# Optimization experiments

Measured on AMD Instinct MI355X. Metric: run time of the kernel, lower is better.

Reference implementation:

```python
import jax, jax.numpy as jnp
import numpy as np

H, W = 256, 192           # cfg.input_img_shape
INF = 9999.0
B, V = 64, 100000


def setup_inputs() -> dict:
    key = jax.random.key(0)
    k1, k2, k3 = jax.random.split(key, 3)
    sdf = jax.random.normal(k1, (B, V), dtype=jnp.float32)
    # pixel coords spanning slightly beyond the image so some verts are invalid
    uv = jax.random.uniform(k2, (B, V, 2), dtype=jnp.float32)
    cloth_meshes = uv * jnp.array([W * 1.1, H * 1.1], jnp.float32) - jnp.array([W * 0.05, H * 0.05], jnp.float32)
    parse_gt = jax.random.randint(k3, (B, H, W), 0, 2).astype(jnp.int32)
    return {
        "sdf": sdf,
        "cloth_meshes": cloth_meshes,
        "parse_gt": parse_gt,
        "sdf_thresh": jnp.ones((1,), jnp.float32),
        "cloth_meshes_unposed": jnp.zeros((1, 1, 3), jnp.float32),
        "parse_valid": jnp.ones((B, 1, 1), jnp.float32),
        "dist_thresh": jnp.ones((1,), jnp.float32),
        "v_template": jnp.zeros((1, 3), jnp.float32),
    }


def reference(sdf, cloth_meshes, parse_gt, sdf_thresh, cloth_meshes_unposed, parse_valid, dist_thresh, v_template):
    b = sdf.shape[0]
    hw = H * W
    x = cloth_meshes[:, :, 0].astype(jnp.int32)
    y = cloth_meshes[:, :, 1].astype(jnp.int32)
    is_valid = (x >= 0) & (x < W) & (y >= 0) & (y < H)
    idx = jnp.where(is_valid, y * W + x, 0)                      # [B,V]
    min_sdf = jnp.where(is_valid, sdf, INF)
    max_sdf = jnp.where(is_valid, sdf, -INF)
    # single flattened segment reduce over B*H*W segments (scatter_min/max)
    flat_idx = (idx + jnp.arange(b, dtype=jnp.int32)[:, None] * hw).reshape(-1)
    pmin = jax.ops.segment_min(min_sdf.reshape(-1), flat_idx, num_segments=b * hw).reshape(b, H, W)
    pmax = jax.ops.segment_max(max_sdf.reshape(-1), flat_idx, num_segments=b * hw).reshape(b, H, W)
    # empty / all-invalid pixels: torch init was +/-INF -> replace
    pmin = jnp.where(pmin >= INF, 0.0, pmin)
    pmax = jnp.where(pmax <= -INF, sdf_thresh[0], pmax)
    pos_mask = (parse_gt == 1).astype(sdf.dtype)
    neg_mask = (parse_gt == 0).astype(sdf.dtype)
    loss_pos = jnp.abs(pmin) * pos_mask * parse_valid
    loss_neg = jnp.abs(pmax - sdf_thresh[0]) * neg_mask * parse_valid
    loss = loss_pos.mean((1, 2)) + loss_neg.mean((1, 2))
    cloth_exist = (pos_mask.sum((1, 2)) > 0).astype(sdf.dtype)
    return loss * cloth_exist
```

## Files before the change

### kernel.cpp

```cpp
#include <hip/hip_runtime.h>


#define HH 256
#define WW 192
#define HW (HH * WW)
#define NB 64
#define NV 100000
#define NS 4
#define RANGE (HW / NS)
#define NC 8
#define CHUNK (NV / NC)
#define F4B (NV / 4 / NC)
#define CAP 3000

__device__ __forceinline__ unsigned fkey(float f) {
    unsigned u = __float_as_uint(f);
    return (u & 0x80000000u) ? ~u : (u | 0x80000000u);
}
__device__ __forceinline__ float funkey(unsigned k) {
    unsigned u = (k & 0x80000000u) ? (k ^ 0x80000000u) : ~k;
    return __uint_as_float(u);
}
__device__ __forceinline__ unsigned key18(float f) {
    unsigned k = fkey(f);
    if (k >= 0xFFFFE000u) return 0x3FFFFu;
    return (k + 0x2000u) >> 14;
}

__global__ __launch_bounds__(512) void bin_kernel(
        const float4* __restrict__ sdf4,
        const float4* __restrict__ mesh4,
        unsigned* __restrict__ cnt,
        unsigned* __restrict__ records) {
    __shared__ unsigned lcur[NS];
    const int b = blockIdx.x >> 3;
    const int c = blockIdx.x & 7;
    const int tid = threadIdx.x;
    if (tid < NS) lcur[tid] = 0;
    __syncthreads();

    const float4* sbase = sdf4  + (size_t)b * (NV / 4) + (size_t)c * F4B;
    const float4* mbase = mesh4 + (size_t)b * (NV / 2) + (size_t)c * F4B * 2;
    unsigned* rbase = records + (size_t)(b * NC + c) * NS * CAP;

    for (int g = tid; g < F4B; g += 512) {
        float4 s4 = sbase[g];
        float4 ma = mbase[2 * g];
        float4 mb = mbase[2 * g + 1];
        float xs[4] = {ma.x, ma.z, mb.x, mb.z};
        float ys[4] = {ma.y, ma.w, mb.y, mb.w};
        float ss[4] = {s4.x, s4.y, s4.z, s4.w};
        #pragma unroll
        for (int j = 0; j < 4; ++j) {
            int x = (int)xs[j];
            int y = (int)ys[j];
            if ((unsigned)x < WW && (unsigned)y < HH) {
                int q = y >> 6;
                unsigned pos = atomicAdd(&lcur[q], 1u);
                if (pos < CAP)
                    rbase[q * CAP + pos] =
                        ((unsigned)((y & 63) * WW + x) << 18) | key18(ss[j]);
            }
        }
    }
    __syncthreads();
    if (tid < NS) cnt[(b * NC + c) * NS + tid] = lcur[tid];
}

__global__ __launch_bounds__(1024) void scatter_reduce_kernel(
        const unsigned* __restrict__ records,
        const unsigned* __restrict__ cnt,
        const int4* __restrict__ gt4,
        const float* __restrict__ thr_p,
        float* __restrict__ sums,
        unsigned* __restrict__ counts) {
    __shared__ unsigned ldsk[RANGE];
    __shared__ unsigned char gtb[RANGE];
    const int b = blockIdx.x >> 2;
    const int q = blockIdx.x & 3;
    const int tid = threadIdx.x;

    int lpos = 0;
    for (int j = tid; j < RANGE; j += 1024) ldsk[j] = 0xFFFFFFFFu;
    const int4* gbase = gt4 + ((size_t)b * HW + (size_t)q * RANGE) / 4;
    for (int j = tid; j < RANGE / 4; j += 1024) {
        int4 g = gbase[j];
        gtb[4 * j + 0] = (unsigned char)g.x;
        gtb[4 * j + 1] = (unsigned char)g.y;
        gtb[4 * j + 2] = (unsigned char)g.z;
        gtb[4 * j + 3] = (unsigned char)g.w;
        lpos |= (g.x == 1) | (g.y == 1) | (g.z == 1) | (g.w == 1);
    }
    __syncthreads();

    for (int c = 0; c < NC; ++c) {
        unsigned n = cnt[(b * NC + c) * NS + q];
        if (n > CAP) n = CAP;
        const unsigned* rb = records + ((size_t)(b * NC + c) * NS + q) * CAP;
        for (unsigned i = tid; i < n; i += 1024) {
            unsigned r = rb[i];
            unsigned p = r >> 18;
            unsigned k = r & 0x3FFFFu;
            if (gtb[p] == 0) k ^= 0x3FFFFu;
            atomicMin(&ldsk[p], k);
        }
    }
    __syncthreads();

    const float thr = thr_p[0];
    float lsum = 0.f;
    for (int j = tid; j < RANGE; j += 1024) {
        unsigned k = ldsk[j];
        if (k <= 0x3FFFFu) {
            if (gtb[j]) lsum += fabsf(funkey(k << 14));
            else        lsum += fabsf(funkey((k ^ 0x3FFFFu) << 14) - thr);
        }
    }
    #pragma unroll
    for (int off = 32; off > 0; off >>= 1)
        lsum += __shfl_down(lsum, off, 64);
    unsigned long long m = __ballot(lpos != 0);
    if ((tid & 63) == 0) {
        atomicAdd(&sums[b], lsum);
        if (m) atomicOr(&counts[b], 1u);
    }
}

__global__ void final_kernel(const float* __restrict__ sums,
                             const unsigned* __restrict__ counts,
                             const float* __restrict__ pv,
                             float* __restrict__ out) {
    int b = threadIdx.x;
    if (b < NB) {
        float s = sums[b] * (1.0f / HW) * pv[b];
        out[b] = counts[b] ? s : 0.0f;
    }
}

extern "C" void kernel_launch(void* const* d_in, const int* in_sizes, int n_in,
                              void* d_out, int out_size, void* d_ws, size_t ws_size,
                              hipStream_t stream) {
    const float* sdf  = (const float*)d_in[0];
    const float* mesh = (const float*)d_in[1];
    const int*   gt   = (const int*)d_in[2];
    const float* thr  = (const float*)d_in[3];
    const float* pv   = (const float*)d_in[5];
    float* out = (float*)d_out;

    unsigned* cnt     = (unsigned*)d_ws;
    float*    sums    = (float*)((char*)d_ws + 8192);
    unsigned* counts  = (unsigned*)((char*)d_ws + 8448);
    unsigned* records = (unsigned*)((char*)d_ws + 8704);

    hipMemsetAsync(sums, 0, 512, stream);

    bin_kernel<<<NB * NC, 512, 0, stream>>>(
        (const float4*)sdf, (const float4*)mesh, cnt, records);

    scatter_reduce_kernel<<<NB * NS, 1024, 0, stream>>>(
        records, cnt, (const int4*)gt, thr, sums, counts);

    final_kernel<<<1, 64, 0, stream>>>(sums, counts, pv, out);
}
```

Measured before the change: 166.2 us.

## Split image into eight row slabs, flatten chunk loop, fold memset into bin kernel

Doubles the number of row slabs, so scatter_reduce runs 512 blocks with half-size LDS tables, and per-slab record capacity is halved to match. The per-chunk loop in the reducer becomes one flat loop over a prefix-summed record count, so all threads stay busy across chunks. The bin kernel now uses 1024 threads per block and zeroes sums/counts itself, which removes the separate memset launch. Smaller CAP raises the risk of overflow, which would silently drop records if a slab is denser than expected.

```diff
diff --git a/kernel.cpp b/kernel.cpp
--- a/kernel.cpp
+++ b/kernel.cpp
@@ -6,12 +6,12 @@
 #define HW (HH * WW)
 #define NB 64
 #define NV 100000
-#define NS 4
+#define NS 8
 #define RANGE (HW / NS)
 #define NC 8
 #define CHUNK (NV / NC)
 #define F4B (NV / 4 / NC)
-#define CAP 3000
+#define CAP 1500
 
 __device__ __forceinline__ unsigned fkey(float f) {
     unsigned u = __float_as_uint(f);
@@ -27,15 +27,22 @@
     return (k + 0x2000u) >> 14;
 }
 
-__global__ __launch_bounds__(512) void bin_kernel(
+__global__ __launch_bounds__(1024) void bin_kernel(
         const float4* __restrict__ sdf4,
         const float4* __restrict__ mesh4,
         unsigned* __restrict__ cnt,
-        unsigned* __restrict__ records) {
+        unsigned* __restrict__ records,
+        float* __restrict__ sums,
+        unsigned* __restrict__ counts) {
     __shared__ unsigned lcur[NS];
     const int b = blockIdx.x >> 3;
     const int c = blockIdx.x & 7;
     const int tid = threadIdx.x;
+
+    if (blockIdx.x == 0) {
+        if (tid < NB) sums[tid] = 0.0f;
+        else if (tid < 2 * NB) counts[tid - NB] = 0u;
+    }
     if (tid < NS) lcur[tid] = 0;
     __syncthreads();
 
@@ -43,7 +50,7 @@
     const float4* mbase = mesh4 + (size_t)b * (NV / 2) + (size_t)c * F4B * 2;
     unsigned* rbase = records + (size_t)(b * NC + c) * NS * CAP;
 
-    for (int g = tid; g < F4B; g += 512) {
+    for (int g = tid; g < F4B; g += 1024) {
         float4 s4 = sbase[g];
         float4 ma = mbase[2 * g];
         float4 mb = mbase[2 * g + 1];
@@ -55,11 +62,11 @@
             int x = (int)xs[j];
             int y = (int)ys[j];
             if ((unsigned)x < WW && (unsigned)y < HH) {
-                int q = y >> 6;
+                int q = y >> 5;
                 unsigned pos = atomicAdd(&lcur[q], 1u);
                 if (pos < CAP)
                     rbase[q * CAP + pos] =
-                        ((unsigned)((y & 63) * WW + x) << 18) | key18(ss[j]);
+                        ((unsigned)((y & 31) * WW + x) << 18) | key18(ss[j]);
             }
         }
     }
@@ -76,8 +83,8 @@
         unsigned* __restrict__ counts) {
     __shared__ unsigned ldsk[RANGE];
     __shared__ unsigned char gtb[RANGE];
-    const int b = blockIdx.x >> 2;
-    const int q = blockIdx.x & 3;
+    const int b = blockIdx.x >> 3;
+    const int q = blockIdx.x & 7;
     const int tid = threadIdx.x;
 
     int lpos = 0;
@@ -93,17 +100,26 @@
     }
     __syncthreads();
 
+    unsigned pref[NC + 1];
+    pref[0] = 0;
+    #pragma unroll
     for (int c = 0; c < NC; ++c) {
         unsigned n = cnt[(b * NC + c) * NS + q];
-        if (n > CAP) n = CAP;
-        const unsigned* rb = records + ((size_t)(b * NC + c) * NS + q) * CAP;
-        for (unsigned i = tid; i < n; i += 1024) {
-            unsigned r = rb[i];
-            unsigned p = r >> 18;
-            unsigned k = r & 0x3FFFFu;
-            if (gtb[p] == 0) k ^= 0x3FFFFu;
-            atomicMin(&ldsk[p], k);
+        pref[c + 1] = pref[c] + (n > CAP ? CAP : n);
+    }
+    const unsigned tot = pref[NC];
+    const unsigned* rq = records + ((size_t)b * NC * NS + q) * CAP;
+    for (unsigned t = tid; t < tot; t += 1024) {
+        unsigned cidx = 0, base = 0;
+        #pragma unroll
+        for (int k = 1; k < NC; ++k) {
+            if (t >= pref[k]) { cidx = k; base = pref[k]; }
         }
+        unsigned r = rq[(size_t)cidx * (NS * CAP) + (t - base)];
+        unsigned p = r >> 18;
+        unsigned k2 = r & 0x3FFFFu;
+        if (gtb[p] == 0) k2 ^= 0x3FFFFu;
+        atomicMin(&ldsk[p], k2);
     }
     __syncthreads();
 
@@ -148,14 +164,12 @@
     float* out = (float*)d_out;
 
     unsigned* cnt     = (unsigned*)d_ws;
-    float*    sums    = (float*)((char*)d_ws + 8192);
-    unsigned* counts  = (unsigned*)((char*)d_ws + 8448);
-    unsigned* records = (unsigned*)((char*)d_ws + 8704);
+    float*    sums    = (float*)((char*)d_ws + 16384);
+    unsigned* counts  = (unsigned*)((char*)d_ws + 16640);
+    unsigned* records = (unsigned*)((char*)d_ws + 16896);
 
-    hipMemsetAsync(sums, 0, 512, stream);
-
-    bin_kernel<<<NB * NC, 512, 0, stream>>>(
-        (const float4*)sdf, (const float4*)mesh, cnt, records);
+    bin_kernel<<<NB * NC, 1024, 0, stream>>>(
+        (const float4*)sdf, (const float4*)mesh, cnt, records, sums, counts);
 
     scatter_reduce_kernel<<<NB * NS, 1024, 0, stream>>>(
         records, cnt, (const int4*)gt, thr, sums, counts);
```

New measurement: 193.1 us. +16.2%, slower.

## Fuse binning, scatter-reduce and finalize into one cooperative kernel with grid syncs

Applied to the files above, without the earlier changes.

Replaces the memset plus three separate kernel launches with a single cooperative kernel of 256 blocks × 1024 threads. Grid-wide syncs separate three phases: binning (each block now handles two chunks), per-quarter scatter-reduce, and the final per-batch output. The scatter phase also reads records as uint4, four at a time, with tail guards. This is meant to remove launch and inter-kernel gap overhead and widen loads, at the cost of grid-sync latency and less parallelism in the binning phase.

```diff
diff --git a/kernel.cpp b/kernel.cpp
--- a/kernel.cpp
+++ b/kernel.cpp
@@ -1,4 +1,7 @@
 #include <hip/hip_runtime.h>
+#include <hip/hip_cooperative_groups.h>
+
+namespace cg = cooperative_groups;
 
 
 #define HH 256
@@ -9,9 +12,10 @@
 #define NS 4
 #define RANGE (HW / NS)
 #define NC 8
-#define CHUNK (NV / NC)
 #define F4B (NV / 4 / NC)
 #define CAP 3000
+#define NBLK 256
+#define NTHR 1024
 
 __device__ __forceinline__ unsigned fkey(float f) {
     unsigned u = __float_as_uint(f);
@@ -27,124 +31,154 @@
     return (k + 0x2000u) >> 14;
 }
 
-__global__ __launch_bounds__(512) void bin_kernel(
+__global__ __launch_bounds__(NTHR) void fused_kernel(
         const float4* __restrict__ sdf4,
         const float4* __restrict__ mesh4,
-        unsigned* __restrict__ cnt,
-        unsigned* __restrict__ records) {
+        const int4*   __restrict__ gt4,
+        const float*  __restrict__ thr_p,
+        const float*  __restrict__ pv,
+        unsigned*     __restrict__ cnt,
+        unsigned*     __restrict__ records,
+        float*        __restrict__ sums,
+        unsigned*     __restrict__ counts,
+        float*        __restrict__ out) {
+    __shared__ unsigned ldsk[RANGE];
+    __shared__ unsigned char gtb[RANGE];
     __shared__ unsigned lcur[NS];
-    const int b = blockIdx.x >> 3;
-    const int c = blockIdx.x & 7;
     const int tid = threadIdx.x;
-    if (tid < NS) lcur[tid] = 0;
-    __syncthreads();
+    const int g = blockIdx.x;
+    cg::grid_group grid = cg::this_grid();
 
-    const float4* sbase = sdf4  + (size_t)b * (NV / 4) + (size_t)c * F4B;
-    const float4* mbase = mesh4 + (size_t)b * (NV / 2) + (size_t)c * F4B * 2;
-    unsigned* rbase = records + (size_t)(b * NC + c) * NS * CAP;
+    if (g == 0) {
+        if (tid < NB) sums[tid] = 0.0f;
+        else if (tid < 2 * NB) counts[tid - NB] = 0u;
+    }
 
-    for (int g = tid; g < F4B; g += 512) {
-        float4 s4 = sbase[g];
-        float4 ma = mbase[2 * g];
-        float4 mb = mbase[2 * g + 1];
-        float xs[4] = {ma.x, ma.z, mb.x, mb.z};
-        float ys[4] = {ma.y, ma.w, mb.y, mb.w};
-        float ss[4] = {s4.x, s4.y, s4.z, s4.w};
-        #pragma unroll
-        for (int j = 0; j < 4; ++j) {
-            int x = (int)xs[j];
-            int y = (int)ys[j];
-            if ((unsigned)x < WW && (unsigned)y < HH) {
-                int q = y >> 6;
-                unsigned pos = atomicAdd(&lcur[q], 1u);
-                if (pos < CAP)
-                    rbase[q * CAP + pos] =
-                        ((unsigned)((y & 63) * WW + x) << 18) | key18(ss[j]);
+    {
+        const int b = g >> 2;
+        const int sub = g & 3;
+        #pragma unroll 1
+        for (int cc = 0; cc < 2; ++cc) {
+            const int c = sub * 2 + cc;
+            if (tid < NS) lcur[tid] = 0;
+            __syncthreads();
+            const float4* sbase = sdf4  + (size_t)b * (NV / 4) + (size_t)c * F4B;
+            const float4* mbase = mesh4 + (size_t)b * (NV / 2) + (size_t)c * F4B * 2;
+            unsigned* rbase = records + (size_t)(b * NC + c) * NS * CAP;
+            for (int gi = tid; gi < F4B; gi += NTHR) {
+                float4 s4 = sbase[gi];
+                float4 ma = mbase[2 * gi];
+                float4 mb = mbase[2 * gi + 1];
+                float xs[4] = {ma.x, ma.z, mb.x, mb.z};
+                float ys[4] = {ma.y, ma.w, mb.y, mb.w};
+                float ss[4] = {s4.x, s4.y, s4.z, s4.w};
+                #pragma unroll
+                for (int j = 0; j < 4; ++j) {
+                    int x = (int)xs[j];
+                    int y = (int)ys[j];
+                    if ((unsigned)x < WW && (unsigned)y < HH) {
+                        int q = y >> 6;
+                        unsigned pos = atomicAdd(&lcur[q], 1u);
+                        if (pos < CAP)
+                            rbase[q * CAP + pos] =
+                                ((unsigned)((y & 63) * WW + x) << 18) | key18(ss[j]);
+                    }
+                }
+            }
+            __syncthreads();
+            if (tid < NS) cnt[(b * NC + c) * NS + tid] = lcur[tid];
+        }
+    }
+
+    __threadfence();
+    grid.sync();
+
+    {
+        const int b = g >> 2;
+        const int q = g & 3;
+
+        int lpos = 0;
+        for (int j = tid; j < RANGE; j += NTHR) ldsk[j] = 0xFFFFFFFFu;
+        const int4* gbase = gt4 + ((size_t)b * HW + (size_t)q * RANGE) / 4;
+        for (int j = tid; j < RANGE / 4; j += NTHR) {
+            int4 gg = gbase[j];
+            gtb[4 * j + 0] = (unsigned char)gg.x;
+            gtb[4 * j + 1] = (unsigned char)gg.y;
+            gtb[4 * j + 2] = (unsigned char)gg.z;
+            gtb[4 * j + 3] = (unsigned char)gg.w;
+            lpos |= (gg.x == 1) | (gg.y == 1) | (gg.z == 1) | (gg.w == 1);
+        }
+        __syncthreads();
+
+        #pragma unroll 1
+        for (int c = 0; c < NC; ++c) {
+            unsigned n = cnt[(b * NC + c) * NS + q];
+            if (n > CAP) n = CAP;
+            const uint4* rb4 = (const uint4*)(records +
+                                   ((size_t)(b * NC + c) * NS + q) * CAP);
+            for (unsigned i = tid; 4 * i < n; i += NTHR) {
+                uint4 r = rb4[i];
+                unsigned rem = n - 4 * i;
+                unsigned p0 = r.x >> 18, k0 = r.x & 0x3FFFFu;
+                unsigned p1 = r.y >> 18, k1 = r.y & 0x3FFFFu;
+                unsigned p2 = r.z >> 18, k2 = r.z & 0x3FFFFu;
+                unsigned p3 = r.w >> 18, k3 = r.w & 0x3FFFFu;
+                if (gtb[p0] == 0) k0 ^= 0x3FFFFu;
+                atomicMin(&ldsk[p0], k0);
+                if (rem > 1) {
+                    if (gtb[p1] == 0) k1 ^= 0x3FFFFu;
+                    atomicMin(&ldsk[p1], k1);
+                }
+                if (rem > 2) {
+                    if (gtb[p2] == 0) k2 ^= 0x3FFFFu;
+                    atomicMin(&ldsk[p2], k2);
+                }
+                if (rem > 3) {
+                    if (gtb[p3] == 0) k3 ^= 0x3FFFFu;
+                    atomicMin(&ldsk[p3], k3);
+                }
             }
         }
-    }
-    __syncthreads();
-    if (tid < NS) cnt[(b * NC + c) * NS + tid] = lcur[tid];
-}
+        __syncthreads();
 
-__global__ __launch_bounds__(1024) void scatter_reduce_kernel(
-        const unsigned* __restrict__ records,
-        const unsigned* __restrict__ cnt,
-        const int4* __restrict__ gt4,
-        const float* __restrict__ thr_p,
-        float* __restrict__ sums,
-        unsigned* __restrict__ counts) {
-    __shared__ unsigned ldsk[RANGE];
-    __shared__ unsigned char gtb[RANGE];
-    const int b = blockIdx.x >> 2;
-    const int q = blockIdx.x & 3;
-    const int tid = threadIdx.x;
-
-    int lpos = 0;
-    for (int j = tid; j < RANGE; j += 1024) ldsk[j] = 0xFFFFFFFFu;
-    const int4* gbase = gt4 + ((size_t)b * HW + (size_t)q * RANGE) / 4;
-    for (int j = tid; j < RANGE / 4; j += 1024) {
-        int4 g = gbase[j];
-        gtb[4 * j + 0] = (unsigned char)g.x;
-        gtb[4 * j + 1] = (unsigned char)g.y;
-        gtb[4 * j + 2] = (unsigned char)g.z;
-        gtb[4 * j + 3] = (unsigned char)g.w;
-        lpos |= (g.x == 1) | (g.y == 1) | (g.z == 1) | (g.w == 1);
-    }
-    __syncthreads();
-
-    for (int c = 0; c < NC; ++c) {
-        unsigned n = cnt[(b * NC + c) * NS + q];
-        if (n > CAP) n = CAP;
-        const unsigned* rb = records + ((size_t)(b * NC + c) * NS + q) * CAP;
-        for (unsigned i = tid; i < n; i += 1024) {
-            unsigned r = rb[i];
-            unsigned p = r >> 18;
-            unsigned k = r & 0x3FFFFu;
-            if (gtb[p] == 0) k ^= 0x3FFFFu;
-            atomicMin(&ldsk[p], k);
+        const float thr = thr_p[0];
+        float lsum = 0.f;
+        for (int j = tid; j < RANGE; j += NTHR) {
+            unsigned k = ldsk[j];
+            if (k <= 0x3FFFFu) {
+                if (gtb[j]) lsum += fabsf(funkey(k << 14));
+                else        lsum += fabsf(funkey((k ^ 0x3FFFFu) << 14) - thr);
+            }
+        }
+        #pragma unroll
+        for (int off = 32; off > 0; off >>= 1)
+            lsum += __shfl_down(lsum, off, 64);
+        unsigned long long m = __ballot(lpos != 0);
+        if ((tid & 63) == 0) {
+            atomicAdd(&sums[b], lsum);
+            if (m) atomicOr(&counts[b], 1u);
         }
     }
-    __syncthreads();
 
-    const float thr = thr_p[0];
-    float lsum = 0.f;
-    for (int j = tid; j < RANGE; j += 1024) {
-        unsigned k = ldsk[j];
-        if (k <= 0x3FFFFu) {
-            if (gtb[j]) lsum += fabsf(funkey(k << 14));
-            else        lsum += fabsf(funkey((k ^ 0x3FFFFu) << 14) - thr);
-        }
-    }
-    #pragma unroll
-    for (int off = 32; off > 0; off >>= 1)
-        lsum += __shfl_down(lsum, off, 64);
-    unsigned long long m = __ballot(lpos != 0);
-    if ((tid & 63) == 0) {
-        atomicAdd(&sums[b], lsum);
-        if (m) atomicOr(&counts[b], 1u);
-    }
-}
+    grid.sync();
 
-__global__ void final_kernel(const float* __restrict__ sums,
-                             const unsigned* __restrict__ counts,
-                             const float* __restrict__ pv,
-                             float* __restrict__ out) {
-    int b = threadIdx.x;
-    if (b < NB) {
-        float s = sums[b] * (1.0f / HW) * pv[b];
-        out[b] = counts[b] ? s : 0.0f;
+    if (g == 0 && tid < NB) {
+        float s = __hip_atomic_load(&sums[tid], __ATOMIC_RELAXED,
+                                    __HIP_MEMORY_SCOPE_AGENT);
+        unsigned cv = __hip_atomic_load(&counts[tid], __ATOMIC_RELAXED,
+                                        __HIP_MEMORY_SCOPE_AGENT);
+        out[tid] = cv ? s * (1.0f / HW) * pv[tid] : 0.0f;
     }
 }
 
 extern "C" void kernel_launch(void* const* d_in, const int* in_sizes, int n_in,
                               void* d_out, int out_size, void* d_ws, size_t ws_size,
                               hipStream_t stream) {
-    const float* sdf  = (const float*)d_in[0];
-    const float* mesh = (const float*)d_in[1];
-    const int*   gt   = (const int*)d_in[2];
-    const float* thr  = (const float*)d_in[3];
-    const float* pv   = (const float*)d_in[5];
+    const float4* sdf4  = (const float4*)d_in[0];
+    const float4* mesh4 = (const float4*)d_in[1];
+    const int4*   gt4   = (const int4*)d_in[2];
+    const float*  thr   = (const float*)d_in[3];
+    const float*  pv    = (const float*)d_in[5];
     float* out = (float*)d_out;
 
     unsigned* cnt     = (unsigned*)d_ws;
@@ -152,13 +186,8 @@
     unsigned* counts  = (unsigned*)((char*)d_ws + 8448);
     unsigned* records = (unsigned*)((char*)d_ws + 8704);
 
-    hipMemsetAsync(sums, 0, 512, stream);
-
-    bin_kernel<<<NB * NC, 512, 0, stream>>>(
-        (const float4*)sdf, (const float4*)mesh, cnt, records);
-
-    scatter_reduce_kernel<<<NB * NS, 1024, 0, stream>>>(
-        records, cnt, (const int4*)gt, thr, sums, counts);
-
-    final_kernel<<<1, 64, 0, stream>>>(sums, counts, pv, out);
+    void* args[] = {&sdf4, &mesh4, &gt4, &thr, &pv,
+                    &cnt, &records, &sums, &counts, &out};
+    hipLaunchCooperativeKernel((void*)fused_kernel, dim3(NBLK), dim3(NTHR),
+                               args, 0, stream);
 }
```

Result: slower. 321.1 us (+93.1%).

## Fuse binning and scatter-reduce into one direct kernel with exact keys

Applied to the files above, without the earlier changes.

Drops the intermediate record-binning pass. Each of the four row-quarter blocks per batch now reads every vertex of its batch directly and does LDS atomicMin on full 32-bit order-preserving keys, instead of on 18-bit quantized keys. Per-block partial sums go to a workspace that the final kernel combines, which removes the global float atomics and the memset. The cost is that sdf and mesh data are read four times per batch, and the design relies on that reuse being served by cache.

```diff
diff --git a/kernel.cpp b/kernel.cpp
--- a/kernel.cpp
+++ b/kernel.cpp
@@ -8,10 +8,7 @@
 #define NV 100000
 #define NS 4
 #define RANGE (HW / NS)
-#define NC 8
-#define CHUNK (NV / NC)
-#define F4B (NV / 4 / NC)
-#define CAP 3000
+#define NTHR 1024
 
 __device__ __forceinline__ unsigned fkey(float f) {
     unsigned u = __float_as_uint(f);
@@ -21,69 +18,26 @@
     unsigned u = (k & 0x80000000u) ? (k ^ 0x80000000u) : ~k;
     return __uint_as_float(u);
 }
-__device__ __forceinline__ unsigned key18(float f) {
-    unsigned k = fkey(f);
-    if (k >= 0xFFFFE000u) return 0x3FFFFu;
-    return (k + 0x2000u) >> 14;
-}
 
-__global__ __launch_bounds__(512) void bin_kernel(
+__global__ __launch_bounds__(NTHR) void direct_kernel(
         const float4* __restrict__ sdf4,
         const float4* __restrict__ mesh4,
-        unsigned* __restrict__ cnt,
-        unsigned* __restrict__ records) {
-    __shared__ unsigned lcur[NS];
-    const int b = blockIdx.x >> 3;
-    const int c = blockIdx.x & 7;
-    const int tid = threadIdx.x;
-    if (tid < NS) lcur[tid] = 0;
-    __syncthreads();
-
-    const float4* sbase = sdf4  + (size_t)b * (NV / 4) + (size_t)c * F4B;
-    const float4* mbase = mesh4 + (size_t)b * (NV / 2) + (size_t)c * F4B * 2;
-    unsigned* rbase = records + (size_t)(b * NC + c) * NS * CAP;
-
-    for (int g = tid; g < F4B; g += 512) {
-        float4 s4 = sbase[g];
-        float4 ma = mbase[2 * g];
-        float4 mb = mbase[2 * g + 1];
-        float xs[4] = {ma.x, ma.z, mb.x, mb.z};
-        float ys[4] = {ma.y, ma.w, mb.y, mb.w};
-        float ss[4] = {s4.x, s4.y, s4.z, s4.w};
-        #pragma unroll
-        for (int j = 0; j < 4; ++j) {
-            int x = (int)xs[j];
-            int y = (int)ys[j];
-            if ((unsigned)x < WW && (unsigned)y < HH) {
-                int q = y >> 6;
-                unsigned pos = atomicAdd(&lcur[q], 1u);
-                if (pos < CAP)
-                    rbase[q * CAP + pos] =
-                        ((unsigned)((y & 63) * WW + x) << 18) | key18(ss[j]);
-            }
-        }
-    }
-    __syncthreads();
-    if (tid < NS) cnt[(b * NC + c) * NS + tid] = lcur[tid];
-}
-
-__global__ __launch_bounds__(1024) void scatter_reduce_kernel(
-        const unsigned* __restrict__ records,
-        const unsigned* __restrict__ cnt,
-        const int4* __restrict__ gt4,
-        const float* __restrict__ thr_p,
-        float* __restrict__ sums,
-        unsigned* __restrict__ counts) {
+        const int4*   __restrict__ gt4,
+        const float*  __restrict__ thr_p,
+        float*        __restrict__ psum,
+        unsigned*     __restrict__ pflag) {
     __shared__ unsigned ldsk[RANGE];
     __shared__ unsigned char gtb[RANGE];
-    const int b = blockIdx.x >> 2;
-    const int q = blockIdx.x & 3;
+    __shared__ float    wsum[16];
+    __shared__ unsigned wflag[16];
+    const int b = blockIdx.x & 63;
+    const int q = blockIdx.x >> 6;
     const int tid = threadIdx.x;
 
     int lpos = 0;
-    for (int j = tid; j < RANGE; j += 1024) ldsk[j] = 0xFFFFFFFFu;
+    for (int j = tid; j < RANGE; j += NTHR) ldsk[j] = 0xFFFFFFFFu;
     const int4* gbase = gt4 + ((size_t)b * HW + (size_t)q * RANGE) / 4;
-    for (int j = tid; j < RANGE / 4; j += 1024) {
+    for (int j = tid; j < RANGE / 4; j += NTHR) {
         int4 g = gbase[j];
         gtb[4 * j + 0] = (unsigned char)g.x;
         gtb[4 * j + 1] = (unsigned char)g.y;
@@ -93,72 +47,82 @@
     }
     __syncthreads();
 
-    for (int c = 0; c < NC; ++c) {
-        unsigned n = cnt[(b * NC + c) * NS + q];
-        if (n > CAP) n = CAP;
-        const unsigned* rb = records + ((size_t)(b * NC + c) * NS + q) * CAP;
-        for (unsigned i = tid; i < n; i += 1024) {
-            unsigned r = rb[i];
-            unsigned p = r >> 18;
-            unsigned k = r & 0x3FFFFu;
-            if (gtb[p] == 0) k ^= 0x3FFFFu;
-            atomicMin(&ldsk[p], k);
+    const float4* sbase = sdf4  + (size_t)b * (NV / 4);
+    const float4* mbase = mesh4 + (size_t)b * (NV / 2);
+    const int qlo = q << 6;
+    for (int gi = tid; gi < NV / 4; gi += NTHR) {
+        float4 s4 = sbase[gi];
+        float4 ma = mbase[2 * gi];
+        float4 mb = mbase[2 * gi + 1];
+        float xs[4] = {ma.x, ma.z, mb.x, mb.z};
+        float ys[4] = {ma.y, ma.w, mb.y, mb.w};
+        float ss[4] = {s4.x, s4.y, s4.z, s4.w};
+        #pragma unroll
+        for (int j = 0; j < 4; ++j) {
+            int x = (int)xs[j];
+            int y = (int)ys[j];
+            if ((unsigned)x < WW && (unsigned)(y - qlo) < 64u) {
+                unsigned p = (unsigned)(y - qlo) * WW + (unsigned)x;
+                unsigned k = fkey(ss[j]);
+                if (gtb[p] == 0) k = ~k;
+                atomicMin(&ldsk[p], k);
+            }
         }
     }
     __syncthreads();
 
     const float thr = thr_p[0];
     float lsum = 0.f;
-    for (int j = tid; j < RANGE; j += 1024) {
+    for (int j = tid; j < RANGE; j += NTHR) {
         unsigned k = ldsk[j];
-        if (k <= 0x3FFFFu) {
-            if (gtb[j]) lsum += fabsf(funkey(k << 14));
-            else        lsum += fabsf(funkey((k ^ 0x3FFFFu) << 14) - thr);
+        if (k != 0xFFFFFFFFu) {
+            if (gtb[j]) lsum += fabsf(funkey(k));
+            else        lsum += fabsf(funkey(~k) - thr);
         }
     }
     #pragma unroll
     for (int off = 32; off > 0; off >>= 1)
         lsum += __shfl_down(lsum, off, 64);
     unsigned long long m = __ballot(lpos != 0);
-    if ((tid & 63) == 0) {
-        atomicAdd(&sums[b], lsum);
-        if (m) atomicOr(&counts[b], 1u);
+    const int wid = tid >> 6;
+    if ((tid & 63) == 0) { wsum[wid] = lsum; wflag[wid] = (m != 0); }
+    __syncthreads();
+    if (tid == 0) {
+        float s = 0.f; unsigned f = 0;
+        #pragma unroll
+        for (int i = 0; i < NTHR / 64; ++i) { s += wsum[i]; f |= wflag[i]; }
+        psum[blockIdx.x]  = s;
+        pflag[blockIdx.x] = f;
     }
 }
 
-__global__ void final_kernel(const float* __restrict__ sums,
-                             const unsigned* __restrict__ counts,
+__global__ void final_kernel(const float* __restrict__ psum,
+                             const unsigned* __restrict__ pflag,
                              const float* __restrict__ pv,
                              float* __restrict__ out) {
     int b = threadIdx.x;
     if (b < NB) {
-        float s = sums[b] * (1.0f / HW) * pv[b];
-        out[b] = counts[b] ? s : 0.0f;
+        float s = psum[b] + psum[NB + b] + psum[2 * NB + b] + psum[3 * NB + b];
+        unsigned f = pflag[b] | pflag[NB + b] | pflag[2 * NB + b] | pflag[3 * NB + b];
+        out[b] = f ? s * (1.0f / HW) * pv[b] : 0.0f;
     }
 }
 
 extern "C" void kernel_launch(void* const* d_in, const int* in_sizes, int n_in,
                               void* d_out, int out_size, void* d_ws, size_t ws_size,
                               hipStream_t stream) {
-    const float* sdf  = (const float*)d_in[0];
-    const float* mesh = (const float*)d_in[1];
-    const int*   gt   = (const int*)d_in[2];
-    const float* thr  = (const float*)d_in[3];
-    const float* pv   = (const float*)d_in[5];
+    const float4* sdf4  = (const float4*)d_in[0];
+    const float4* mesh4 = (const float4*)d_in[1];
+    const int4*   gt4   = (const int4*)d_in[2];
+    const float*  thr   = (const float*)d_in[3];
+    const float*  pv    = (const float*)d_in[5];
     float* out = (float*)d_out;
 
-    unsigned* cnt     = (unsigned*)d_ws;
-    float*    sums    = (float*)((char*)d_ws + 8192);
-    unsigned* counts  = (unsigned*)((char*)d_ws + 8448);
-    unsigned* records = (unsigned*)((char*)d_ws + 8704);
+    float*    psum  = (float*)d_ws;
+    unsigned* pflag = (unsigned*)((char*)d_ws + 1024);
 
-    hipMemsetAsync(sums, 0, 512, stream);
+    direct_kernel<<<NS * NB, NTHR, 0, stream>>>(
+        sdf4, mesh4, gt4, thr, psum, pflag);
 
-    bin_kernel<<<NB * NC, 512, 0, stream>>>(
-        (const float4*)sdf, (const float4*)mesh, cnt, records);
-
-    scatter_reduce_kernel<<<NB * NS, 1024, 0, stream>>>(
-        records, cnt, (const int4*)gt, thr, sums, counts);
-
-    final_kernel<<<1, 64, 0, stream>>>(sums, counts, pv, out);
+    final_kernel<<<1, 64, 0, stream>>>(psum, pflag, pv, out);
 }
```

After: 155.1 us. -6.7%, faster.
